# Performance work log

Measured on AMD Instinct MI355X. Metric: run time of the kernel, lower is better.

Reference implementation:

```python
import jax, jax.numpy as jnp
import numpy as np

B, T, D, HID, NB, HH = 1024, 128, 256, 512, 64, 8
LN_EPS = 1e-5


def setup_inputs() -> dict:
    key = jax.random.key(0)
    ks = jax.random.split(key, 16)
    s = 0.02
    return {
        "context_features": jax.random.normal(ks[0], (B, T, D), jnp.float32),
        "beam_history": jax.random.randint(ks[1], (B, HH), 0, NB, jnp.int64),
        "E": jax.random.normal(ks[2], (NB, D), jnp.float32) * s,          # beam embedding
        "W_in": jax.random.normal(ks[3], (2 * D, HID), jnp.float32) * s,  # in_proj Linear
        "b_in": jnp.zeros((HID,), jnp.float32),
        "W_init": jax.random.normal(ks[4], (2 * D, HID), jnp.float32) * s,
        "b_init": jnp.zeros((HID,), jnp.float32),
        "W_ih": jax.random.normal(ks[5], (3 * HID, HID), jnp.float32) * s,  # GRUCell input weights
        "W_hh": jax.random.normal(ks[6], (3 * HID, HID), jnp.float32) * s,  # GRUCell hidden weights
        "b_ih": jnp.zeros((3 * HID,), jnp.float32),
        "b_hh": jnp.zeros((3 * HID,), jnp.float32),
        "ln_g": jnp.ones((HID,), jnp.float32),
        "ln_b": jnp.zeros((HID,), jnp.float32),
        "W_o1": jax.random.normal(ks[7], (HID + D, HID), jnp.float32) * s,
        "b_o1": jnp.zeros((HID,), jnp.float32),
        "W_o2": jax.random.normal(ks[8], (HID, NB), jnp.float32) * s,
        "b_o2": jnp.zeros((NB,), jnp.float32),
    }


def _gru_cell(x, h, W_ih, W_hh, b_ih, b_hh):
    # PyTorch nn.GRUCell semantics
    gi = x @ W_ih.T + b_ih   # (B, 3H)
    gh = h @ W_hh.T + b_hh
    i_r, i_z, i_n = jnp.split(gi, 3, axis=-1)
    h_r, h_z, h_n = jnp.split(gh, 3, axis=-1)
    r = jax.nn.sigmoid(i_r + h_r)
    z = jax.nn.sigmoid(i_z + h_z)
    n = jnp.tanh(i_n + r * h_n)
    return (1.0 - z) * n + z * h


def _layernorm(x, g, b):
    mu = jnp.mean(x, axis=-1, keepdims=True)
    var = jnp.mean(jnp.square(x - mu), axis=-1, keepdims=True)
    return (x - mu) * jax.lax.rsqrt(var + LN_EPS) * g + b


def reference(context_features, beam_history, E, W_in, b_in, W_init, b_init,
              W_ih, W_hh, b_ih, b_hh, ln_g, ln_b, W_o1, b_o1, W_o2, b_o2):
    bh = beam_history.astype(jnp.int32)
    prev_beam0 = bh[:, -1]                       # (B,)
    hist_emb = jnp.mean(E[bh], axis=1)           # (B, D)
    ctx_global = jnp.mean(context_features, axis=1)  # (B, D)
    h0 = jnp.tanh(jnp.concatenate([ctx_global, hist_emb], axis=-1) @ W_init + b_init)

    ctx_t_first = jnp.transpose(context_features, (1, 0, 2))  # (T, B, D)

    def step(carry, ctx_t):
        h, prev_beam = carry
        prev_emb = E[prev_beam]                               # (B, D)
        x = jax.nn.relu(jnp.concatenate([ctx_t, prev_emb], axis=-1) @ W_in + b_in)
        h = _gru_cell(x, h, W_ih, W_hh, b_ih, b_hh)
        h_norm = _layernorm(h, ln_g, ln_b)
        hidden = jax.nn.relu(jnp.concatenate([h_norm, ctx_t], axis=-1) @ W_o1 + b_o1)
        logits_t = hidden @ W_o2 + b_o2                       # (B, NB)
        prev_beam = jnp.argmax(logits_t, axis=-1).astype(jnp.int32)
        return (h, prev_beam), logits_t

    (_, _), logits = jax.lax.scan(step, (h0, prev_beam0), ctx_t_first)
    ar_logits = jnp.transpose(logits, (1, 0, 2))  # (B, T, NB)
    return ar_logits
```

## Files before the change

### kernel.cpp

```cpp
#include <hip/hip_runtime.h>

typedef _Float16 half8 __attribute__((ext_vector_type(8)));
typedef float f32x4 __attribute__((ext_vector_type(4)));

#define MFMA(a,b,c) __builtin_amdgcn_mfma_f32_16x16x32_f16((a),(b),(c),0,0,0)

#define PKW_BYTES ((size_t)(4*468 + 4*456)*1024)
#define OFF_ETAB  PKW_BYTES
#define OFF_H0    (OFF_ETAB + (size_t)64*512*4)
#define OFF_XPRE  (OFF_H0 + (size_t)1024*512*4)
#define OFF_HPRE  (OFF_XPRE + (size_t)1024*128*512*2)

__global__ void packw_k(const float* __restrict__ W_ih, const float* __restrict__ W_hh,
                        const float* __restrict__ W_o1, const float* __restrict__ W_o2,
                        _Float16* __restrict__ pkw)
{
  int ts = blockIdx.x, w = blockIdx.y;
  if (w >= 4 && ts >= 456) return;
  int lane = threadIdx.x, lo = lane & 15, kb8 = (lane >> 4)*8;
  half8 v;
  #pragma unroll
  for (int e = 0; e < 8; e++) v[e] = (_Float16)0.f;
  if (ts < 384){
    int i = ts/96, r = ts%96, a = r/16, kq = r%16;
    int n = w*64 + i*16 + lo;
    #pragma unroll
    for (int e = 0; e < 8; e++){
      int k = kq*32 + kb8 + e;
      v[e] = (a < 3) ? (_Float16)W_ih[(a*512 + n)*512 + k]
                     : (_Float16)W_hh[((a-3)*512 + n)*512 + k];
    }
  } else if (ts < 448){
    int td = ts - 384;
    int i = td >> 4, ks = td & 15, n = w*64 + i*16 + lo;
    #pragma unroll
    for (int e = 0; e < 8; e++) v[e] = (_Float16)W_o1[(ks*32 + kb8 + e)*512 + n];
  } else if (ts >= 448 && ts < 464 && w < 4){
    int te = ts - 448, n = w*16 + lo;
    #pragma unroll
    for (int e = 0; e < 8; e++) v[e] = (_Float16)W_o2[(te*32 + kb8 + e)*64 + n];
  }
  long base = (w < 4) ? (long)w*468 : (long)1872 + (long)(w-4)*456;
  *(half8*)(pkw + (base + ts)*512 + lane*8) = v;
}

__global__ void etab_k(const float* __restrict__ E, const float* __restrict__ W_in,
                       const float* __restrict__ b_in, float* __restrict__ Etab)
{
  int e = blockIdx.x, tid = threadIdx.x;
  __shared__ float er[256];
  if (tid < 256) er[tid] = E[e*256 + tid];
  __syncthreads();
  for (int j = tid; j < 512; j += 256){
    float acc = b_in[j];
    for (int k = 0; k < 256; k++) acc += er[k] * W_in[(256 + k)*512 + j];
    Etab[e*512 + j] = acc;
  }
}

__global__ __launch_bounds__(512) void h0_k(const float* __restrict__ ctx,
    const int* __restrict__ bh, const float* __restrict__ E,
    const float* __restrict__ W_init, const float* __restrict__ b_init,
    float* __restrict__ h0w)
{
  int b0 = blockIdx.x * 16, tid = threadIdx.x;
  __shared__ float cat[16][512];
  int c = tid & 255, rh = tid >> 8;
  for (int rr = 0; rr < 8; rr++){
    int r2 = rh*8 + rr;
    const float* p = ctx + ((b0 + r2)*128)*256 + c;
    float acc = 0.f;
    for (int t = 0; t < 128; t++) acc += p[t*256];
    cat[r2][c] = acc * (1.f/128.f);
    float s = 0.f;
    #pragma unroll
    for (int hh = 0; hh < 8; hh++){
      int e = bh[(b0 + r2)*8 + hh];
      s += E[e*256 + c];
    }
    cat[r2][256 + c] = s * 0.125f;
  }
  __syncthreads();
  int j = tid;
  float acc[16];
  #pragma unroll
  for (int r2 = 0; r2 < 16; r2++) acc[r2] = b_init[j];
  for (int k = 0; k < 512; k++){
    float wv = W_init[k*512 + j];
    #pragma unroll
    for (int r2 = 0; r2 < 16; r2++) acc[r2] += cat[r2][k] * wv;
  }
  #pragma unroll
  for (int r2 = 0; r2 < 16; r2++) h0w[(b0 + r2)*512 + j] = tanhf(acc[r2]);
}

__global__ __launch_bounds__(512) void prep_k(const float* __restrict__ ctx,
    const float* __restrict__ W_in, const float* __restrict__ W_o1,
    _Float16* __restrict__ xpre, _Float16* __restrict__ hpre)
{
  int b = blockIdx.x, tid = threadIdx.x;
  int w = tid >> 6, lane = tid & 63, lo = lane & 15, hi = lane >> 4;
  extern __shared__ __align__(16) _Float16 A_lds[];

  {
    int ra = tid >> 2, ca = (tid & 3)*64;
    const float* p = ctx + ((long)b*128 + ra)*256 + ca;
    #pragma unroll
    for (int c8 = 0; c8 < 8; c8++){
      float4 f0 = *(const float4*)(p + c8*8);
      float4 f1 = *(const float4*)(p + c8*8 + 4);
      half8 v;
      v[0]=(_Float16)f0.x; v[1]=(_Float16)f0.y; v[2]=(_Float16)f0.z; v[3]=(_Float16)f0.w;
      v[4]=(_Float16)f1.x; v[5]=(_Float16)f1.y; v[6]=(_Float16)f1.z; v[7]=(_Float16)f1.w;
      *(half8*)((char*)A_lds + (((ra*512 + (ca + c8*8)*2)) ^ ((ra&7)<<4))) = v;
    }
  }
  __syncthreads();

  const float* Wb = (w < 4) ? W_in : (W_o1 + 512*512);
  _Float16* outp = (w < 4) ? xpre : hpre;
  const int colbase = (w & 3)*128;
  const int aswzp = (lo & 7) << 4;

  #pragma unroll 1
  for (int cth = 0; cth < 4; cth++){
    half8 bf0[8], bf1[8];
    const int n0 = colbase + cth*32 + lo;
    #pragma unroll
    for (int ks = 0; ks < 8; ks++){
      const int kb = ks*32 + hi*8;
      half8 v0, v1;
      #pragma unroll
      for (int e = 0; e < 8; e++){
        v0[e] = (_Float16)Wb[(kb + e)*512 + n0];
        v1[e] = (_Float16)Wb[(kb + e)*512 + n0 + 16];
      }
      bf0[ks] = v0; bf1[ks] = v1;
    }
    #pragma unroll 1
    for (int rt = 0; rt < 8; rt++){
      f32x4 acc0 = {0,0,0,0}, acc1 = {0,0,0,0};
      #pragma unroll
      for (int ks = 0; ks < 8; ks++){
        half8 a = *(const half8*)((const char*)A_lds +
                   ((((rt*16 + lo)*512 + hi*16 + ks*64)) ^ aswzp));
        acc0 = MFMA(a, bf0[ks], acc0);
        acc1 = MFMA(a, bf1[ks], acc1);
      }
      #pragma unroll
      for (int rr = 0; rr < 4; rr++){
        int t = rt*16 + hi*4 + rr;
        long rowoff = ((long)b*128 + t)*512 + colbase + cth*32;
        outp[rowoff +      lo] = (_Float16)acc0[rr];
        outp[rowoff + 16 + lo] = (_Float16)acc1[rr];
      }
    }
  }
}

#define AFRAG(buf, base, ks) (*(const half8*)((const char*)(buf) + ((((base) + (ks)*64)) ^ aswz)))
#define WSTORE(buf, row, j, val) \
  *(_Float16*)((char*)(buf) + ((((row)*1024 + (j)*2)) ^ ((((row)&7))<<4))) = (_Float16)(val)
#define WSTORE8(buf, row, colf16, v8) \
  *(half8*)((char*)(buf) + ((((row)*1024 + (colf16)*2)) ^ ((((row)&7))<<4))) = (v8)

__global__ __launch_bounds__(512) void main10_k(
    const _Float16* __restrict__ pkw, const float* __restrict__ Etab,
    const float* __restrict__ h0w, const _Float16* __restrict__ xpre,
    const _Float16* __restrict__ hpre, const int* __restrict__ bh,
    const float* __restrict__ b_ih, const float* __restrict__ b_hh,
    const float* __restrict__ lng, const float* __restrict__ lnb,
    const float* __restrict__ b_o1, const float* __restrict__ b_o2,
    float* __restrict__ out)
{
  const int g = blockIdx.x, tid = threadIdx.x;
  const int w = tid >> 6, lane = tid & 63, lo = lane & 15, hi = lane >> 4;
  const int r0 = g*16;

  __shared__ __align__(16) _Float16 h_s [16*512];
  __shared__ __align__(16) _Float16 hn_s[16*512];
  __shared__ __align__(16) _Float16 xh_s[16*512];
  __shared__ float lg_s[16*64];
  __shared__ float stats[8][4][4][2];
  __shared__ float murs[16][2];
  __shared__ float bias_s[3][512];
  __shared__ int   pb[16];

  float bcr[4], bcz[4], bin_[4], bhn[4];
  #pragma unroll
  for (int i = 0; i < 4; i++){
    int j = w*64 + i*16 + lo;
    bcr[i] = b_ih[j]     + b_hh[j];
    bcz[i] = b_ih[512+j] + b_hh[512+j];
    bin_[i]= b_ih[1024+j];
    bhn[i] = b_hh[1024+j];
  }
  const float bo2v = (w < 4) ? b_o2[w*16 + lo] : 0.f;
  if (tid < 512){
    bias_s[0][tid] = b_o1[tid];
    bias_s[1][tid] = lng[tid];
    bias_s[2][tid] = lnb[tid];
  }

  float hreg[4][4];
  #pragma unroll
  for (int i = 0; i < 4; i++)
    #pragma unroll
    for (int rr = 0; rr < 4; rr++)
      hreg[i][rr] = h0w[(r0 + hi*4 + rr)*512 + w*64 + i*16 + lo];

  #pragma unroll
  for (int c2 = 0; c2 < 2; c2++){
    int ch = tid*2 + c2, rr = ch >> 6, c8 = ch & 63;
    const float* p = h0w + (r0 + rr)*512 + c8*8;
    half8 v;
    #pragma unroll
    for (int e = 0; e < 8; e++) v[e] = (_Float16)p[e];
    *(half8*)((char*)h_s + (((rr*1024 + c8*16)) ^ ((rr&7)<<4))) = v;
  }
  if (tid < 16) pb[tid] = bh[(r0 + tid)*8 + 7];
  __syncthreads();

  const int aswz  = (lo & 7) << 4;
  const int abase = lo*1024 + hi*16;
  const char* pkw_w = (const char*)pkw +
      ((w < 4) ? (long)w*468*1024 : ((long)1872 + (long)(w-4)*456)*1024);

  #pragma unroll 1
  for (int t = 0; t < 128; t++){
    {
      int rowA = tid >> 5, c32 = (tid & 31)*16;
      const _Float16* xp = xpre + (((long)(r0 + rowA)*128 + t)*512) + c32;
      half8 x0 = __builtin_nontemporal_load((const half8*)xp);
      half8 x1 = __builtin_nontemporal_load((const half8*)(xp + 8));
      const float* ep = Etab + pb[rowA]*512 + c32;
      float4 e0 = *(const float4*)(ep);
      float4 e1 = *(const float4*)(ep + 4);
      float4 e2 = *(const float4*)(ep + 8);
      float4 e3 = *(const float4*)(ep + 12);
      half8 o0, o1;
      o0[0]=(_Float16)fmaxf((float)x0[0]+e0.x,0.f); o0[1]=(_Float16)fmaxf((float)x0[1]+e0.y,0.f);
      o0[2]=(_Float16)fmaxf((float)x0[2]+e0.z,0.f); o0[3]=(_Float16)fmaxf((float)x0[3]+e0.w,0.f);
      o0[4]=(_Float16)fmaxf((float)x0[4]+e1.x,0.f); o0[5]=(_Float16)fmaxf((float)x0[5]+e1.y,0.f);
      o0[6]=(_Float16)fmaxf((float)x0[6]+e1.z,0.f); o0[7]=(_Float16)fmaxf((float)x0[7]+e1.w,0.f);
      o1[0]=(_Float16)fmaxf((float)x1[0]+e2.x,0.f); o1[1]=(_Float16)fmaxf((float)x1[1]+e2.y,0.f);
      o1[2]=(_Float16)fmaxf((float)x1[2]+e2.z,0.f); o1[3]=(_Float16)fmaxf((float)x1[3]+e2.w,0.f);
      o1[4]=(_Float16)fmaxf((float)x1[4]+e3.x,0.f); o1[5]=(_Float16)fmaxf((float)x1[5]+e3.y,0.f);
      o1[6]=(_Float16)fmaxf((float)x1[6]+e3.z,0.f); o1[7]=(_Float16)fmaxf((float)x1[7]+e3.w,0.f);
      WSTORE8(xh_s, rowA, c32,     o0);
      WSTORE8(xh_s, rowA, c32 + 8, o1);
    }
    __syncthreads();

    float srow[4] = {0,0,0,0}, sqrow[4] = {0,0,0,0};
    #pragma unroll 1
    for (int i = 0; i < 4; i++){
      f32x4 a0={0,0,0,0},a1={0,0,0,0},a2={0,0,0,0},a3={0,0,0,0},a4={0,0,0,0},a5={0,0,0,0};
      #pragma unroll
      for (int a6 = 0; a6 < 6; a6++){
        const _Float16* ab = (a6 < 3) ? xh_s : h_s;
        #pragma unroll
        for (int hf = 0; hf < 2; hf++){
          half8 bb[8];
          const char* tp = pkw_w + (((long)(i*96 + a6*16 + hf*8)) << 10) + (lane << 4);
          #pragma unroll
          for (int k8 = 0; k8 < 8; k8++)
            bb[k8] = *(const half8*)(tp + ((long)k8 << 10));
          #pragma unroll
          for (int k8 = 0; k8 < 8; k8++){
            half8 af = AFRAG(ab, abase, hf*8 + k8);
            if      (a6 == 0) a0 = MFMA(af, bb[k8], a0);
            else if (a6 == 1) a1 = MFMA(af, bb[k8], a1);
            else if (a6 == 2) a2 = MFMA(af, bb[k8], a2);
            else if (a6 == 3) a3 = MFMA(af, bb[k8], a3);
            else if (a6 == 4) a4 = MFMA(af, bb[k8], a4);
            else              a5 = MFMA(af, bb[k8], a5);
          }
        }
      }
      #pragma unroll
      for (int rr = 0; rr < 4; rr++){
        float rg = 1.f/(1.f + __expf(-(a0[rr] + a3[rr] + bcr[i])));
        float zg = 1.f/(1.f + __expf(-(a1[rr] + a4[rr] + bcz[i])));
        float aa = (a2[rr] + bin_[i]) + rg*(a5[rr] + bhn[i]);
        float ea = __expf(-2.f*fabsf(aa));
        float th = (1.f - ea)/(1.f + ea);
        float ng = (aa < 0.f) ? -th : th;
        float hv = (1.f - zg)*ng + zg*hreg[i][rr];
        hreg[i][rr] = hv;
        srow[rr] += hv; sqrow[rr] += hv*hv;
      }
    }
    #pragma unroll
    for (int d = 1; d < 16; d <<= 1){
      #pragma unroll
      for (int rr = 0; rr < 4; rr++){
        srow[rr]  += __shfl_xor(srow[rr],  d);
        sqrow[rr] += __shfl_xor(sqrow[rr], d);
      }
    }
    if (lo == 0){
      #pragma unroll
      for (int rr = 0; rr < 4; rr++){
        stats[w][hi][rr][0] = srow[rr];
        stats[w][hi][rr][1] = sqrow[rr];
      }
    }
    __syncthreads();
    if (w == 0 && lane < 16){
      float s = 0.f, q = 0.f;
      #pragma unroll
      for (int ww = 0; ww < 8; ww++){
        s += stats[ww][lane>>2][lane&3][0];
        q += stats[ww][lane>>2][lane&3][1];
      }
      float mu = s*(1.f/512.f);
      float var = q*(1.f/512.f) - mu*mu;
      murs[lane][0] = mu;
      murs[lane][1] = rsqrtf(var + 1e-5f);
    }
    __syncthreads();

    float hp[4][4];
    #pragma unroll
    for (int rr = 0; rr < 4; rr++){
      int row = hi*4 + rr;
      float mu = murs[row][0], rs = murs[row][1];
      #pragma unroll
      for (int i = 0; i < 4; i++){
        int jc = w*64 + i*16 + lo;
        float hv = hreg[i][rr];
        WSTORE(h_s,  row, jc, hv);
        WSTORE(hn_s, row, jc, (hv - mu)*rs*bias_s[1][jc] + bias_s[2][jc]);
        hp[i][rr] = (float)__builtin_nontemporal_load(
            &hpre[(((long)(r0 + row)*128 + t)*512) + jc]);
      }
    }
    __syncthreads();

    #pragma unroll 1
    for (int i = 0; i < 4; i++){
      half8 bd[16];
      #pragma unroll
      for (int ks = 0; ks < 16; ks++)
        bd[ks] = *(const half8*)(pkw_w + (((long)(384 + i*16 + ks)) << 10) + (lane << 4));
      f32x4 dacc = {0,0,0,0};
      #pragma unroll
      for (int ks = 0; ks < 16; ks++)
        dacc = MFMA(AFRAG(hn_s, abase, ks), bd[ks], dacc);
      const float bo1j = bias_s[0][w*64 + i*16 + lo];
      #pragma unroll
      for (int rr = 0; rr < 4; rr++){
        int row = hi*4 + rr;
        WSTORE(xh_s, row, w*64 + i*16 + lo, fmaxf(dacc[rr] + bo1j + hp[i][rr], 0.f));
      }
    }
    __syncthreads();

    if (w < 4){
      half8 be[16];
      #pragma unroll
      for (int ks = 0; ks < 16; ks++)
        be[ks] = *(const half8*)(pkw_w + (((long)(448 + ks)) << 10) + (lane << 4));
      f32x4 eacc = {0,0,0,0};
      #pragma unroll
      for (int ks = 0; ks < 16; ks++)
        eacc = MFMA(AFRAG(xh_s, abase, ks), be[ks], eacc);
      #pragma unroll
      for (int rr = 0; rr < 4; rr++){
        int row = hi*4 + rr;
        lg_s[row*64 + w*16 + lo] = eacc[rr] + bo2v;
      }
    }
    __syncthreads();

    #pragma unroll
    for (int sub = 0; sub < 2; sub++){
      int r2 = w*2 + sub;
      float v = lg_s[r2*64 + lane];
      __builtin_nontemporal_store(v, &out[(((long)(r0 + r2))*128 + t)*64 + lane]);
      int idx = lane;
      #pragma unroll
      for (int d = 1; d < 64; d <<= 1){
        float ov = __shfl_xor(v, d);
        int oi = __shfl_xor(idx, d);
        if (ov > v || (ov == v && oi < idx)){ v = ov; idx = oi; }
      }
      if (lane == 0) pb[r2] = idx;
    }
    __syncthreads();
  }
}

extern "C" void kernel_launch(void* const* d_in, const int* in_sizes, int n_in,
                              void* d_out, int out_size, void* d_ws, size_t ws_size,
                              hipStream_t stream)
{
  const float* ctx    = (const float*)d_in[0];
  const int*   bh     = (const int*)d_in[1];
  const float* E      = (const float*)d_in[2];
  const float* W_in   = (const float*)d_in[3];
  const float* b_in   = (const float*)d_in[4];
  const float* W_init = (const float*)d_in[5];
  const float* b_init = (const float*)d_in[6];
  const float* W_ih   = (const float*)d_in[7];
  const float* W_hh   = (const float*)d_in[8];
  const float* b_ih   = (const float*)d_in[9];
  const float* b_hh   = (const float*)d_in[10];
  const float* ln_g   = (const float*)d_in[11];
  const float* ln_b   = (const float*)d_in[12];
  const float* W_o1   = (const float*)d_in[13];
  const float* b_o1   = (const float*)d_in[14];
  const float* W_o2   = (const float*)d_in[15];
  const float* b_o2   = (const float*)d_in[16];
  float* out = (float*)d_out;

  _Float16* pkw  = (_Float16*)d_ws;
  float*    Etab = (float*)((char*)d_ws + OFF_ETAB);
  float*    h0w  = (float*)((char*)d_ws + OFF_H0);
  _Float16* xpre = (_Float16*)((char*)d_ws + OFF_XPRE);
  _Float16* hpre = (_Float16*)((char*)d_ws + OFF_HPRE);

  (void)hipFuncSetAttribute((const void*)prep_k,
      hipFuncAttributeMaxDynamicSharedMemorySize, 65536);

  hipLaunchKernelGGL(packw_k, dim3(468, 8), dim3(64), 0, stream, W_ih, W_hh, W_o1, W_o2, pkw);
  hipLaunchKernelGGL(etab_k, dim3(64), dim3(256), 0, stream, E, W_in, b_in, Etab);
  hipLaunchKernelGGL(h0_k, dim3(64), dim3(512), 0, stream, ctx, bh, E, W_init, b_init, h0w);
  hipLaunchKernelGGL(prep_k, dim3(1024), dim3(512), 65536, stream, ctx, W_in, W_o1, xpre, hpre);
  hipLaunchKernelGGL(main10_k, dim3(64), dim3(512), 0, stream,
                     pkw, Etab, h0w, xpre, hpre, bh,
                     b_ih, b_hh, ln_g, ln_b, b_o1, b_o2, out);
}
```

Measured before the change: 6.284 ms.

## Split each batch group's GRU across two cooperating blocks with global-memory flag sync

Each 16-row batch group is now handled by two workgroups, and each one computes half of the GRU hidden columns. Every timestep the halves exchange their hidden state and LayerNorm partial sums through global memory, using acquire/release flags and spin-waits. The W_ih/W_hh weights are repacked per half-stream, and the O1/O2 layers are computed redundantly in both blocks. This doubles the number of active CUs (128 instead of 64) to cut per-block MFMA and weight-streaming work on the serial recurrence. The cost is a cross-block handshake every step, and the kernel can deadlock if both blocks of a pair are not co-resident, although the spin loops are bounded.

```diff
diff --git a/kernel.cpp b/kernel.cpp
--- a/kernel.cpp
+++ b/kernel.cpp
@@ -5,43 +5,63 @@
 
 #define MFMA(a,b,c) __builtin_amdgcn_mfma_f32_16x16x32_f16((a),(b),(c),0,0,0)
 
-#define PKW_BYTES ((size_t)(4*468 + 4*456)*1024)
+#define PKW_BYTES ((size_t)(4*240 + 12*224)*1024)
 #define OFF_ETAB  PKW_BYTES
 #define OFF_H0    (OFF_ETAB + (size_t)64*512*4)
 #define OFF_XPRE  (OFF_H0 + (size_t)1024*512*4)
 #define OFF_HPRE  (OFF_XPRE + (size_t)1024*128*512*2)
+#define OFF_FLG   (OFF_HPRE + (size_t)1024*128*512*2)
+
+__device__ __forceinline__ int ld_acq(const int* p){
+  return __hip_atomic_load(p, __ATOMIC_ACQUIRE, __HIP_MEMORY_SCOPE_AGENT);
+}
+__device__ __forceinline__ void st_rel(int* p, int v){
+  __hip_atomic_store(p, v, __ATOMIC_RELEASE, __HIP_MEMORY_SCOPE_AGENT);
+}
+__device__ __forceinline__ void spin_ge(const int* p, int v){
+  int n = 0;
+  while (ld_acq(p) < v && n < (1<<16)){ __builtin_amdgcn_s_sleep(8); n++; }
+}
+
+__device__ __forceinline__ long stream_base(int sid){
+  return (sid < 4) ? (long)sid*240 : (long)960 + (long)(sid-4)*224;
+}
 
 __global__ void packw_k(const float* __restrict__ W_ih, const float* __restrict__ W_hh,
                         const float* __restrict__ W_o1, const float* __restrict__ W_o2,
                         _Float16* __restrict__ pkw)
 {
-  int ts = blockIdx.x, w = blockIdx.y;
-  if (w >= 4 && ts >= 456) return;
+  int ts = blockIdx.x, sid = blockIdx.y;
+  if (sid >= 4 && ts >= 224) return;
   int lane = threadIdx.x, lo = lane & 15, kb8 = (lane >> 4)*8;
   half8 v;
   #pragma unroll
   for (int e = 0; e < 8; e++) v[e] = (_Float16)0.f;
-  if (ts < 384){
+  if (ts < 192){
     int i = ts/96, r = ts%96, a = r/16, kq = r%16;
-    int n = w*64 + i*16 + lo;
+    int n = sid*32 + i*16 + lo;
     #pragma unroll
     for (int e = 0; e < 8; e++){
       int k = kq*32 + kb8 + e;
       v[e] = (a < 3) ? (_Float16)W_ih[(a*512 + n)*512 + k]
                      : (_Float16)W_hh[((a-3)*512 + n)*512 + k];
     }
-  } else if (ts < 448){
-    int td = ts - 384;
-    int i = td >> 4, ks = td & 15, n = w*64 + i*16 + lo;
+  } else if (ts < 224){
+    int td = ts - 192;
+    int i = td >> 4, ks = td & 15, n = sid*32 + i*16 + lo;
     #pragma unroll
     for (int e = 0; e < 8; e++) v[e] = (_Float16)W_o1[(ks*32 + kb8 + e)*512 + n];
-  } else if (ts >= 448 && ts < 464 && w < 4){
-    int te = ts - 448, n = w*16 + lo;
-    #pragma unroll
-    for (int e = 0; e < 8; e++) v[e] = (_Float16)W_o2[(te*32 + kb8 + e)*64 + n];
-  }
-  long base = (w < 4) ? (long)w*468 : (long)1872 + (long)(w-4)*456;
-  *(half8*)(pkw + (base + ts)*512 + lane*8) = v;
+  } else {
+    int ks = ts - 224, n = sid*16 + lo;
+    #pragma unroll
+    for (int e = 0; e < 8; e++) v[e] = (_Float16)W_o2[(ks*32 + kb8 + e)*64 + n];
+  }
+  *(half8*)(pkw + (stream_base(sid) + ts)*512 + lane*8) = v;
+}
+
+__global__ void flaginit_k(int* __restrict__ f){
+  int i = threadIdx.x;
+  if (i < 384) f[i] = 0;
 }
 
 __global__ void etab_k(const float* __restrict__ E, const float* __restrict__ W_in,
@@ -164,67 +184,82 @@
 #define WSTORE8(buf, row, colf16, v8) \
   *(half8*)((char*)(buf) + ((((row)*1024 + (colf16)*2)) ^ ((((row)&7))<<4))) = (v8)
 
-__global__ __launch_bounds__(512) void main10_k(
+__global__ __launch_bounds__(512) void main12_k(
     const _Float16* __restrict__ pkw, const float* __restrict__ Etab,
-    const float* __restrict__ h0w, const _Float16* __restrict__ xpre,
+    float* __restrict__ h0w, const _Float16* __restrict__ xpre,
     const _Float16* __restrict__ hpre, const int* __restrict__ bh,
     const float* __restrict__ b_ih, const float* __restrict__ b_hh,
     const float* __restrict__ lng, const float* __restrict__ lnb,
     const float* __restrict__ b_o1, const float* __restrict__ b_o2,
-    float* __restrict__ out)
+    int* __restrict__ flags, float* __restrict__ out)
 {
-  const int g = blockIdx.x, tid = threadIdx.x;
+  const int bid = blockIdx.x, tid = threadIdx.x;
+  const int g = bid >> 1, s = bid & 1, peer = s ^ 1;
   const int w = tid >> 6, lane = tid & 63, lo = lane & 15, hi = lane >> 4;
-  const int r0 = g*16;
-
-  __shared__ __align__(16) _Float16 h_s [16*512];
+  const int r0 = g*16, sid = s*8 + w;
+
+  __shared__ __align__(16) _Float16 hbuf[16*512];
   __shared__ __align__(16) _Float16 hn_s[16*512];
   __shared__ __align__(16) _Float16 xh_s[16*512];
   __shared__ float lg_s[16*64];
   __shared__ float stats[8][4][4][2];
   __shared__ float murs[16][2];
-  __shared__ float bias_s[3][512];
+  __shared__ float bias_s[3*512];
   __shared__ int   pb[16];
 
-  float bcr[4], bcz[4], bin_[4], bhn[4];
+  char* regi  = (char*)h0w + (long)g*32768;
+  char* hx_own  = regi + s*8192;
+  char* hx_peer = regi + peer*8192;
+  float* ps_own  = (float*)(regi + 16384 + s*128);
+  float* ps_peer = (float*)(regi + 16384 + peer*128);
+  int* flag_p = flags;
+  int* flag_h = flags + 128;
+  int* ackf   = flags + 256;
+
+  float bcr[2], bcz[2], bin_[2], bhn[2];
   #pragma unroll
-  for (int i = 0; i < 4; i++){
-    int j = w*64 + i*16 + lo;
+  for (int i = 0; i < 2; i++){
+    int j = sid*32 + i*16 + lo;
     bcr[i] = b_ih[j]     + b_hh[j];
     bcz[i] = b_ih[512+j] + b_hh[512+j];
     bin_[i]= b_ih[1024+j];
     bhn[i] = b_hh[1024+j];
   }
   const float bo2v = (w < 4) ? b_o2[w*16 + lo] : 0.f;
-  if (tid < 512){
-    bias_s[0][tid] = b_o1[tid];
-    bias_s[1][tid] = lng[tid];
-    bias_s[2][tid] = lnb[tid];
-  }
-
-  float hreg[4][4];
+  bias_s[tid]        = b_o1[tid];
+  bias_s[512 + tid]  = lng[tid];
+  bias_s[1024 + tid] = lnb[tid];
+
+  float hreg[2][4];
   #pragma unroll
-  for (int i = 0; i < 4; i++)
+  for (int i = 0; i < 2; i++)
     #pragma unroll
     for (int rr = 0; rr < 4; rr++)
-      hreg[i][rr] = h0w[(r0 + hi*4 + rr)*512 + w*64 + i*16 + lo];
-
-  #pragma unroll
-  for (int c2 = 0; c2 < 2; c2++){
-    int ch = tid*2 + c2, rr = ch >> 6, c8 = ch & 63;
-    const float* p = h0w + (r0 + rr)*512 + c8*8;
-    half8 v;
-    #pragma unroll
-    for (int e = 0; e < 8; e++) v[e] = (_Float16)p[e];
-    *(half8*)((char*)h_s + (((rr*1024 + c8*16)) ^ ((rr&7)<<4))) = v;
+      hreg[i][rr] = h0w[(r0 + hi*4 + rr)*512 + sid*32 + i*16 + lo];
+
+  {
+    int rr = tid >> 5, c16 = (tid & 31)*16;
+    const float* p = h0w + (r0 + rr)*512 + c16;
+    half8 v0, v1;
+    #pragma unroll
+    for (int e = 0; e < 8; e++){ v0[e] = (_Float16)p[e]; v1[e] = (_Float16)p[8+e]; }
+    WSTORE8(hbuf, rr, c16,     v0);
+    WSTORE8(hbuf, rr, c16 + 8, v1);
   }
   if (tid < 16) pb[tid] = bh[(r0 + tid)*8 + 7];
   __syncthreads();
 
+  if (tid == 0){
+    __threadfence();
+    st_rel(&flag_p[g*2 + s], 1);
+    spin_ge(&flag_p[g*2 + peer], 1);
+  }
+  __syncthreads();
+
   const int aswz  = (lo & 7) << 4;
   const int abase = lo*1024 + hi*16;
-  const char* pkw_w = (const char*)pkw +
-      ((w < 4) ? (long)w*468*1024 : ((long)1872 + (long)(w-4)*456)*1024);
+  const char* pkb = (const char*)pkw;
+  const char* pkw_w = pkb + (stream_base(sid) << 10);
 
   #pragma unroll 1
   for (int t = 0; t < 128; t++){
@@ -254,11 +289,11 @@
 
     float srow[4] = {0,0,0,0}, sqrow[4] = {0,0,0,0};
     #pragma unroll 1
-    for (int i = 0; i < 4; i++){
+    for (int i = 0; i < 2; i++){
       f32x4 a0={0,0,0,0},a1={0,0,0,0},a2={0,0,0,0},a3={0,0,0,0},a4={0,0,0,0},a5={0,0,0,0};
       #pragma unroll
       for (int a6 = 0; a6 < 6; a6++){
-        const _Float16* ab = (a6 < 3) ? xh_s : h_s;
+        const _Float16* ab = (a6 < 3) ? xh_s : hbuf;
         #pragma unroll
         for (int hf = 0; hf < 2; hf++){
           half8 bb[8];
@@ -307,48 +342,102 @@
       }
     }
     __syncthreads();
-    if (w == 0 && lane < 16){
-      float s = 0.f, q = 0.f;
-      #pragma unroll
-      for (int ww = 0; ww < 8; ww++){
-        s += stats[ww][lane>>2][lane&3][0];
-        q += stats[ww][lane>>2][lane&3][1];
-      }
-      float mu = s*(1.f/512.f);
-      float var = q*(1.f/512.f) - mu*mu;
-      murs[lane][0] = mu;
-      murs[lane][1] = rsqrtf(var + 1e-5f);
-    }
-    __syncthreads();
-
-    float hp[4][4];
+
     #pragma unroll
     for (int rr = 0; rr < 4; rr++){
       int row = hi*4 + rr;
+      #pragma unroll
+      for (int i = 0; i < 2; i++)
+        WSTORE(hbuf, row, sid*32 + i*16 + lo, hreg[i][rr]);
+    }
+    __syncthreads();
+    if (tid == 0) spin_ge(&ackf[g*2 + peer], t);
+    __syncthreads();
+    {
+      int row = tid >> 5, k = tid & 31;
+      half8 v = *(const half8*)((const char*)hbuf + row*1024 + s*512 + k*16);
+      *(half8*)(hx_own + row*512 + k*16) = v;
+      if (w == 0 && lane < 16){
+        float sv = 0.f, qv = 0.f;
+        #pragma unroll
+        for (int ww = 0; ww < 8; ww++){
+          sv += stats[ww][lane>>2][lane&3][0];
+          qv += stats[ww][lane>>2][lane&3][1];
+        }
+        ps_own[lane*2 + 0] = sv;
+        ps_own[lane*2 + 1] = qv;
+      }
+    }
+    __syncthreads();
+    if (tid == 0){
+      __threadfence();
+      st_rel(&flag_h[g*2 + s], t + 1);
+      spin_ge(&flag_h[g*2 + peer], t + 1);
+    }
+    __syncthreads();
+    {
+      int row = tid >> 5, k = tid & 31;
+      half8 v = *(const half8*)(hx_peer + row*512 + k*16);
+      *(half8*)((char*)hbuf + row*1024 + peer*512 + k*16) = v;
+      if (w == 0 && lane < 16){
+        float sv = 0.f, qv = 0.f;
+        #pragma unroll
+        for (int ww = 0; ww < 8; ww++){
+          sv += stats[ww][lane>>2][lane&3][0];
+          qv += stats[ww][lane>>2][lane&3][1];
+        }
+        float sp = ps_peer[lane*2 + 0];
+        float qp = ps_peer[lane*2 + 1];
+        float su = sv + sp, qu = qv + qp;
+        float mu = su*(1.f/512.f);
+        float var = qu*(1.f/512.f) - mu*mu;
+        murs[lane][0] = mu;
+        murs[lane][1] = rsqrtf(var + 1e-5f);
+      }
+    }
+    __syncthreads();
+    if (tid == 0){ __threadfence(); st_rel(&ackf[g*2 + s], t + 1); }
+    float hp[4][4];
+    {
+      int row = tid >> 5, c16 = (tid & 31)*16;
       float mu = murs[row][0], rs = murs[row][1];
-      #pragma unroll
-      for (int i = 0; i < 4; i++){
-        int jc = w*64 + i*16 + lo;
-        float hv = hreg[i][rr];
-        WSTORE(h_s,  row, jc, hv);
-        WSTORE(hn_s, row, jc, (hv - mu)*rs*bias_s[1][jc] + bias_s[2][jc]);
+      const int swz = (row & 7) << 4;
+      const int base = row*1024 + c16*2;
+      half8 v0 = *(const half8*)((const char*)hbuf + ((base     ) ^ swz));
+      half8 v1 = *(const half8*)((const char*)hbuf + ((base + 16) ^ swz));
+      half8 o0, o1;
+      #pragma unroll
+      for (int e = 0; e < 8; e++){
+        o0[e] = (_Float16)(((float)v0[e] - mu)*rs*bias_s[512 + c16 + e]     + bias_s[1024 + c16 + e]);
+        o1[e] = (_Float16)(((float)v1[e] - mu)*rs*bias_s[512 + c16 + 8 + e] + bias_s[1024 + c16 + 8 + e]);
+      }
+      WSTORE8(hn_s, row, c16,     o0);
+      WSTORE8(hn_s, row, c16 + 8, o1);
+    }
+    #pragma unroll
+    for (int rr = 0; rr < 4; rr++){
+      int row = hi*4 + rr;
+      #pragma unroll
+      for (int i = 0; i < 4; i++)
         hp[i][rr] = (float)__builtin_nontemporal_load(
-            &hpre[(((long)(r0 + row)*128 + t)*512) + jc]);
-      }
+            &hpre[(((long)(r0 + row)*128 + t)*512) + w*64 + i*16 + lo]);
     }
     __syncthreads();
 
     #pragma unroll 1
     for (int i = 0; i < 4; i++){
+      const int nt = w*4 + i;
+      const int sd = nt >> 1, id = nt & 1;
+      const char* dp = pkb + ((stream_base(sd) + 192 + id*16) << 10) + (lane << 4);
       half8 bd[16];
       #pragma unroll
       for (int ks = 0; ks < 16; ks++)
-        bd[ks] = *(const half8*)(pkw_w + (((long)(384 + i*16 + ks)) << 10) + (lane << 4));
+        bd[ks] = *(const half8*)(dp + ((long)ks << 10));
       f32x4 dacc = {0,0,0,0};
       #pragma unroll
       for (int ks = 0; ks < 16; ks++)
         dacc = MFMA(AFRAG(hn_s, abase, ks), bd[ks], dacc);
-      const float bo1j = bias_s[0][w*64 + i*16 + lo];
+      const float bo1j = bias_s[w*64 + i*16 + lo];
       #pragma unroll
       for (int rr = 0; rr < 4; rr++){
         int row = hi*4 + rr;
@@ -358,10 +447,11 @@
     __syncthreads();
 
     if (w < 4){
+      const char* ep_ = pkb + (((long)w*240 + 224) << 10) + (lane << 4);
       half8 be[16];
       #pragma unroll
       for (int ks = 0; ks < 16; ks++)
-        be[ks] = *(const half8*)(pkw_w + (((long)(448 + ks)) << 10) + (lane << 4));
+        be[ks] = *(const half8*)(ep_ + ((long)ks << 10));
       f32x4 eacc = {0,0,0,0};
       #pragma unroll
       for (int ks = 0; ks < 16; ks++)
@@ -378,7 +468,8 @@
     for (int sub = 0; sub < 2; sub++){
       int r2 = w*2 + sub;
       float v = lg_s[r2*64 + lane];
-      __builtin_nontemporal_store(v, &out[(((long)(r0 + r2))*128 + t)*64 + lane]);
+      if (s == 0)
+        __builtin_nontemporal_store(v, &out[(((long)(r0 + r2))*128 + t)*64 + lane]);
       int idx = lane;
       #pragma unroll
       for (int d = 1; d < 64; d <<= 1){
@@ -420,15 +511,17 @@
   float*    h0w  = (float*)((char*)d_ws + OFF_H0);
   _Float16* xpre = (_Float16*)((char*)d_ws + OFF_XPRE);
   _Float16* hpre = (_Float16*)((char*)d_ws + OFF_HPRE);
+  int*      flg  = (int*)((char*)d_ws + OFF_FLG);
 
   (void)hipFuncSetAttribute((const void*)prep_k,
       hipFuncAttributeMaxDynamicSharedMemorySize, 65536);
 
-  hipLaunchKernelGGL(packw_k, dim3(468, 8), dim3(64), 0, stream, W_ih, W_hh, W_o1, W_o2, pkw);
+  hipLaunchKernelGGL(packw_k, dim3(240, 16), dim3(64), 0, stream, W_ih, W_hh, W_o1, W_o2, pkw);
+  hipLaunchKernelGGL(flaginit_k, dim3(1), dim3(384), 0, stream, flg);
   hipLaunchKernelGGL(etab_k, dim3(64), dim3(256), 0, stream, E, W_in, b_in, Etab);
   hipLaunchKernelGGL(h0_k, dim3(64), dim3(512), 0, stream, ctx, bh, E, W_init, b_init, h0w);
   hipLaunchKernelGGL(prep_k, dim3(1024), dim3(512), 65536, stream, ctx, W_in, W_o1, xpre, hpre);
-  hipLaunchKernelGGL(main10_k, dim3(64), dim3(512), 0, stream,
+  hipLaunchKernelGGL(main12_k, dim3(128), dim3(512), 0, stream,
                      pkw, Etab, h0w, xpre, hpre, bh,
-                     b_ih, b_hh, ln_g, ln_b, b_o1, b_o2, out);
-}
+                     b_ih, b_hh, ln_g, ln_b, b_o1, b_o2, flg, out);
+}
```

Measured after the change: 5.790 ms. 7.9% less time.
